# Optimization experiments

Measured on AMD Instinct MI355X. Metric: run time of the kernel, lower is better.

## Reference

```python
import jax, jax.numpy as jnp
import numpy as np

DMODEL = 1024
NHEADS = 16
FFN = 4 * DMODEL
HEAD_DIM = DMODEL // NHEADS
SCALE = HEAD_DIM ** -0.5


def layer_norm(x, gamma, beta, eps=1e-5):
    mu = jnp.mean(x, axis=-1, keepdims=True)
    var = jnp.var(x, axis=-1, keepdims=True)
    return (x - mu) * jax.lax.rsqrt(var + eps) * gamma + beta


def setup_inputs() -> dict:
    key = jax.random.key(0)
    ks = jax.random.split(key, 8)
    std = 0.02
    B, S = 2, 2048
    return {
        "src": jax.random.normal(ks[0], (B, S, DMODEL), jnp.float32),
        "pre_gamma": jnp.ones((DMODEL,), jnp.float32),
        "pre_beta": jnp.zeros((DMODEL,), jnp.float32),
        "qkv_w": jax.random.truncated_normal(ks[1], -2.0, 2.0, (3 * DMODEL, DMODEL), jnp.float32) * std,
        "qkv_b": jnp.zeros((3 * DMODEL,), jnp.float32),
        "addnorm_gamma": jnp.ones((DMODEL,), jnp.float32),
        "addnorm_beta": jnp.zeros((DMODEL,), jnp.float32),
        "fc1_w": jax.random.truncated_normal(ks[2], -2.0, 2.0, (FFN, DMODEL), jnp.float32) * std,
        "fc1_b": jnp.zeros((FFN,), jnp.float32),
        "fc2_w": jax.random.truncated_normal(ks[3], -2.0, 2.0, (DMODEL, FFN), jnp.float32) * std,
        "fc2_b": jnp.zeros((DMODEL,), jnp.float32),
    }


def reference(src, pre_gamma, pre_beta, qkv_w, qkv_b, addnorm_gamma, addnorm_beta,
              fc1_w, fc1_b, fc2_w, fc2_b):
    B, S, D = src.shape
    # PreNorm
    x = layer_norm(src, pre_gamma, pre_beta)
    # MHSA (no output projection, matching source)
    qkv = x @ qkv_w.T + qkv_b  # [B,S,3D]
    q, k, v = jnp.split(qkv, 3, axis=-1)
    def heads(t):
        return t.reshape(B, S, NHEADS, HEAD_DIM).transpose(0, 2, 1, 3)  # [B,H,S,hd]
    q, k, v = heads(q), heads(k), heads(v)
    attn = jnp.einsum("bhqd,bhkd->bhqk", q, k) * SCALE
    attn = jax.nn.softmax(attn, axis=-1)
    attn_out = jnp.einsum("bhqk,bhkd->bhqd", attn, v)
    attn_out = attn_out.transpose(0, 2, 1, 3).reshape(B, S, D)
    # shared AddNorm #1
    x = layer_norm(attn_out + x, addnorm_gamma, addnorm_beta)
    # FFN
    h = jax.nn.gelu(x @ fc1_w.T + fc1_b, approximate=False)
    ffn_out = h @ fc2_w.T + fc2_b
    # shared AddNorm #2 (same params as #1)
    return layer_norm(ffn_out + x, addnorm_gamma, addnorm_beta)
```

## Files before the change

kernel.cpp:

```cpp
#include <hip/hip_runtime.h>
#include <hip/hip_bf16.h>
#include <math.h>

#define DMODEL 1024
#define NH 16
#define HD 64
#define SEQ 2048
#define BATCH 2
#define MROWS (BATCH * SEQ)
#define FFN_DIM 4096

using bf16x8 = __attribute__((ext_vector_type(8))) __bf16;
using f32x4  = __attribute__((ext_vector_type(4))) float;

typedef const __attribute__((address_space(1))) unsigned char* gas_t;
typedef __attribute__((address_space(3))) unsigned char* las_t;

__device__ inline unsigned short f2bf(float f) {
    unsigned int u = __builtin_bit_cast(unsigned int, f);
    u += 0x7fffu + ((u >> 16) & 1u);
    return (unsigned short)(u >> 16);
}
__device__ inline unsigned short f2bf_up(float f) {
    unsigned int u = __builtin_bit_cast(unsigned int, f);
    return (unsigned short)((u + 0x8000u) >> 16);
}
__device__ inline float bf2f(unsigned short u) {
    unsigned int v = ((unsigned int)u) << 16;
    return __builtin_bit_cast(float, v);
}
__device__ inline float gelu_f(float x) {
    float x2 = x * x;
    float w = x * fmaf(0.07135481627f, x2, 1.59576912161f);
    return x / (1.0f + __expf(-w));
}

__global__ __launch_bounds__(256) void ln_pre_cvt(
        const float* __restrict__ a,
        const float* __restrict__ gamma, const float* __restrict__ beta,
        float* __restrict__ out_f, unsigned short* __restrict__ out_b,
        const float* __restrict__ wa, unsigned short* __restrict__ oa, int na4,
        const float* __restrict__ wb, unsigned short* __restrict__ ob, int nb4,
        const float* __restrict__ wc, unsigned char* __restrict__ oc, int nc4) {
    int blk = blockIdx.x;
    int t = threadIdx.x;
    if (blk >= MROWS) {
        int i = (blk - MROWS) * 256 + t;
        if (i < na4) {
            float4 v = ((const float4*)wa)[i];
            ushort4 o;
            o.x = f2bf(v.x); o.y = f2bf(v.y); o.z = f2bf(v.z); o.w = f2bf(v.w);
            ((ushort4*)oa)[i] = o;
        } else if (i < na4 + nb4) {
            int j = i - na4;
            float4 v = ((const float4*)wb)[j];
            ushort4 o;
            o.x = f2bf(v.x); o.y = f2bf(v.y); o.z = f2bf(v.z); o.w = f2bf(v.w);
            ((ushort4*)ob)[j] = o;
        } else if (i < na4 + nb4 + nc4) {
            int j = i - na4 - nb4;
            float4 v = ((const float4*)wc)[j];
            int pk = __builtin_amdgcn_cvt_pk_fp8_f32(v.x, v.y, 0, false);
            pk     = __builtin_amdgcn_cvt_pk_fp8_f32(v.z, v.w, pk, true);
            ((unsigned int*)oc)[j] = (unsigned int)pk;
        }
        return;
    }
    int row = blk;
    float4 v = ((const float4*)(a + (size_t)row * DMODEL))[t];
    float s  = v.x + v.y + v.z + v.w;
    float s2 = v.x * v.x + v.y * v.y + v.z * v.z + v.w * v.w;
    #pragma unroll
    for (int off = 32; off > 0; off >>= 1) {
        s  += __shfl_xor(s,  off, 64);
        s2 += __shfl_xor(s2, off, 64);
    }
    __shared__ float red[8];
    int wave = t >> 6, lane = t & 63;
    if (lane == 0) { red[wave] = s; red[4 + wave] = s2; }
    __syncthreads();
    float tot  = red[0] + red[1] + red[2] + red[3];
    float tot2 = red[4] + red[5] + red[6] + red[7];
    float mu   = tot * (1.0f / DMODEL);
    float var  = tot2 * (1.0f / DMODEL) - mu * mu;
    float rstd = rsqrtf(var + 1e-5f);
    float4 g  = ((const float4*)gamma)[t];
    float4 be = ((const float4*)beta)[t];
    float4 o;
    o.x = (v.x - mu) * rstd * g.x + be.x;
    o.y = (v.y - mu) * rstd * g.y + be.y;
    o.z = (v.z - mu) * rstd * g.z + be.z;
    o.w = (v.w - mu) * rstd * g.w + be.w;
    ((float4*)(out_f + (size_t)row * DMODEL))[t] = o;
    ushort4 ob4;
    ob4.x = f2bf(o.x); ob4.y = f2bf(o.y); ob4.z = f2bf(o.z); ob4.w = f2bf(o.w);
    ((ushort4*)(out_b + (size_t)row * DMODEL))[t] = ob4;
}

__global__ __launch_bounds__(256) void ln_attn(
        const float* __restrict__ o0, const float* __restrict__ o1,
        const float* __restrict__ l0, const float* __restrict__ l1,
        const float* __restrict__ xres,
        const float* __restrict__ gamma, const float* __restrict__ beta,
        float* __restrict__ out_f, unsigned short* __restrict__ out_b) {
    int row = blockIdx.x;
    int t = threadIdx.x;
    int b_ = row >> 11, s = row & 2047;
    int h = t >> 4;
    int bh = b_ * NH + h;
    size_t obase = ((size_t)bh * SEQ + s) * HD + (4 * t & 63);
    float4 va = ((const float4*)(o0 + obase))[0];
    float4 vb = ((const float4*)(o1 + obase))[0];
    float inv_l = 1.0f / (l0[(size_t)bh * SEQ + s] + l1[(size_t)bh * SEQ + s]);
    float4 rr = ((const float4*)(xres + (size_t)row * DMODEL))[t];
    float4 v;
    v.x = (va.x + vb.x) * inv_l + rr.x;
    v.y = (va.y + vb.y) * inv_l + rr.y;
    v.z = (va.z + vb.z) * inv_l + rr.z;
    v.w = (va.w + vb.w) * inv_l + rr.w;

    float s1 = v.x + v.y + v.z + v.w;
    float s2 = v.x * v.x + v.y * v.y + v.z * v.z + v.w * v.w;
    #pragma unroll
    for (int off = 32; off > 0; off >>= 1) {
        s1 += __shfl_xor(s1, off, 64);
        s2 += __shfl_xor(s2, off, 64);
    }
    __shared__ float red[8];
    int wave = t >> 6, lane = t & 63;
    if (lane == 0) { red[wave] = s1; red[4 + wave] = s2; }
    __syncthreads();
    float tot  = red[0] + red[1] + red[2] + red[3];
    float tot2 = red[4] + red[5] + red[6] + red[7];
    float mu   = tot * (1.0f / DMODEL);
    float var  = tot2 * (1.0f / DMODEL) - mu * mu;
    float rstd = rsqrtf(var + 1e-5f);
    float4 g  = ((const float4*)gamma)[t];
    float4 be = ((const float4*)beta)[t];
    float4 o;
    o.x = (v.x - mu) * rstd * g.x + be.x;
    o.y = (v.y - mu) * rstd * g.y + be.y;
    o.z = (v.z - mu) * rstd * g.z + be.z;
    o.w = (v.w - mu) * rstd * g.w + be.w;
    ((float4*)(out_f + (size_t)row * DMODEL))[t] = o;
    ushort4 ob;
    ob.x = f2bf(o.x); ob.y = f2bf(o.y); ob.z = f2bf(o.z); ob.w = f2bf(o.w);
    ((ushort4*)(out_b + (size_t)row * DMODEL))[t] = ob;
}

__global__ __launch_bounds__(256) void ln_fc2(
        const unsigned short* __restrict__ p0, const unsigned short* __restrict__ p1,
        const unsigned short* __restrict__ p2, const unsigned short* __restrict__ p3,
        const float* __restrict__ bias, const float* __restrict__ resid,
        const float* __restrict__ gamma, const float* __restrict__ beta,
        float* __restrict__ out_f) {
    int row = blockIdx.x;
    int t = threadIdx.x;
    size_t base = (size_t)row * DMODEL;
    ushort4 u0 = ((const ushort4*)(p0 + base))[t];
    ushort4 u1 = ((const ushort4*)(p1 + base))[t];
    ushort4 u2 = ((const ushort4*)(p2 + base))[t];
    ushort4 u3 = ((const ushort4*)(p3 + base))[t];
    float4 bb = ((const float4*)bias)[t];
    float4 rr = ((const float4*)(resid + base))[t];
    float4 v;
    v.x = bf2f(u0.x) + bf2f(u1.x) + bf2f(u2.x) + bf2f(u3.x) + bb.x + rr.x;
    v.y = bf2f(u0.y) + bf2f(u1.y) + bf2f(u2.y) + bf2f(u3.y) + bb.y + rr.y;
    v.z = bf2f(u0.z) + bf2f(u1.z) + bf2f(u2.z) + bf2f(u3.z) + bb.z + rr.z;
    v.w = bf2f(u0.w) + bf2f(u1.w) + bf2f(u2.w) + bf2f(u3.w) + bb.w + rr.w;

    float s  = v.x + v.y + v.z + v.w;
    float s2 = v.x * v.x + v.y * v.y + v.z * v.z + v.w * v.w;
    #pragma unroll
    for (int off = 32; off > 0; off >>= 1) {
        s  += __shfl_xor(s,  off, 64);
        s2 += __shfl_xor(s2, off, 64);
    }
    __shared__ float red[8];
    int wave = t >> 6, lane = t & 63;
    if (lane == 0) { red[wave] = s; red[4 + wave] = s2; }
    __syncthreads();
    float tot  = red[0] + red[1] + red[2] + red[3];
    float tot2 = red[4] + red[5] + red[6] + red[7];
    float mu   = tot * (1.0f / DMODEL);
    float var  = tot2 * (1.0f / DMODEL) - mu * mu;
    float rstd = rsqrtf(var + 1e-5f);
    float4 g  = ((const float4*)gamma)[t];
    float4 be = ((const float4*)beta)[t];
    float4 o;
    o.x = (v.x - mu) * rstd * g.x + be.x;
    o.y = (v.y - mu) * rstd * g.y + be.y;
    o.z = (v.z - mu) * rstd * g.z + be.z;
    o.w = (v.w - mu) * rstd * g.w + be.w;
    ((float4*)(out_f + base))[t] = o;
}

template <int MODE>
__global__ __launch_bounds__(256) void gemm_lds(
        const unsigned short* __restrict__ A,
        const unsigned short* __restrict__ Bw,
        const float* __restrict__ bias,
        void* __restrict__ out, int M, int N, int K) {
    __shared__ unsigned short As[2][128 * 64];
    __shared__ unsigned short Bs[2][128 * 64];

    const int tid  = threadIdx.x;
    const int wave = tid >> 6;
    const int lane = tid & 63;
    const int quad = lane >> 4;
    const int cc   = lane & 15;
    const int bn = blockIdx.x * 128;
    const int bm = blockIdx.y * 128;

    const unsigned short* Ab = A  + (size_t)bm * K;
    const unsigned short* Bb = Bw + (size_t)bn * K;

    const int srow0 = tid >> 3;
    const int sslot = tid & 7;
    const int rsw   = (cc >> 1) & 7;
    const int wm = (wave >> 1) * 64;
    const int wn = (wave & 1) * 64;

    f32x4 acc[4][4] = {};

    auto stage = [&](int buf, int k0) {
        #pragma unroll
        for (int i = 0; i < 4; ++i) {
            int row = i * 32 + srow0;
            int g   = sslot ^ ((row >> 1) & 7);
            const unsigned short* ga = Ab + (size_t)row * K + k0 + g * 8;
            const unsigned short* gb = Bb + (size_t)row * K + k0 + g * 8;
            unsigned short* la = &As[buf][i * 2048 + wave * 512];
            unsigned short* lb = &Bs[buf][i * 2048 + wave * 512];
            __builtin_amdgcn_global_load_lds((gas_t)(const void*)ga, (las_t)(void*)la, 16, 0, 0);
            __builtin_amdgcn_global_load_lds((gas_t)(const void*)gb, (las_t)(void*)lb, 16, 0, 0);
        }
    };

    const int nkt = K >> 6;
    stage(0, 0);
    __syncthreads();

    int cur = 0;
    for (int kt = 0; kt < nkt; ++kt) {
        if (kt + 1 < nkt) stage(cur ^ 1, (kt + 1) << 6);

        bf16x8 af[4][2], bf[4][2];
        #pragma unroll
        for (int mt = 0; mt < 4; ++mt)
            #pragma unroll
            for (int s = 0; s < 2; ++s) {
                int slot = (s * 4 + quad) ^ rsw;
                af[mt][s] = *(const bf16x8*)&As[cur][(wm + mt * 16 + cc) * 64 + slot * 8];
            }
        #pragma unroll
        for (int nt = 0; nt < 4; ++nt)
            #pragma unroll
            for (int s = 0; s < 2; ++s) {
                int slot = (s * 4 + quad) ^ rsw;
                bf[nt][s] = *(const bf16x8*)&Bs[cur][(wn + nt * 16 + cc) * 64 + slot * 8];
            }

        #pragma unroll
        for (int mt = 0; mt < 4; ++mt)
            #pragma unroll
            for (int nt = 0; nt < 4; ++nt) {
                acc[mt][nt] = __builtin_amdgcn_mfma_f32_16x16x32_bf16(
                    af[mt][0], bf[nt][0], acc[mt][nt], 0, 0, 0);
                acc[mt][nt] = __builtin_amdgcn_mfma_f32_16x16x32_bf16(
                    af[mt][1], bf[nt][1], acc[mt][nt], 0, 0, 0);
            }

        if (kt + 1 < nkt) __syncthreads();
        cur ^= 1;
    }

    #pragma unroll
    for (int mt = 0; mt < 4; ++mt)
        #pragma unroll
        for (int nt = 0; nt < 4; ++nt) {
            if constexpr (MODE == 1) {
                int m0 = bm + wm + mt * 16 + quad * 4;
                int n  = bn + wn + nt * 16 + cc;
                float bn_ = bias[n];
                float v0 = gelu_f(acc[mt][nt][0] + bn_);
                float v1 = gelu_f(acc[mt][nt][1] + bn_);
                float v2 = gelu_f(acc[mt][nt][2] + bn_);
                float v3 = gelu_f(acc[mt][nt][3] + bn_);
                int pk = __builtin_amdgcn_cvt_pk_fp8_f32(v0, v1, 0, false);
                pk     = __builtin_amdgcn_cvt_pk_fp8_f32(v2, v3, pk, true);
                unsigned char* o = (unsigned char*)out + (size_t)m0 * N + n;
                o[0]             = (unsigned char)pk;
                o[(size_t)N]     = (unsigned char)(pk >> 8);
                o[(size_t)2 * N] = (unsigned char)(pk >> 16);
                o[(size_t)3 * N] = (unsigned char)(pk >> 24);
            } else {
                #pragma unroll
                for (int r = 0; r < 4; ++r) {
                    int m = bm + wm + mt * 16 + quad * 4 + r;
                    int n = bn + wn + nt * 16 + cc;
                    float v = acc[mt][nt][r] + bias[n];
                    int b_ = m >> 11, srow = m & 2047;
                    int which = n >> 10, rem = n & 1023;
                    int h = rem >> 6, d = rem & 63;
                    if (which == 0) v *= 0.125f;
                    size_t idx = ((((size_t)which * BATCH + b_) * NH + h) * SEQ + srow) * HD + d;
                    ((unsigned short*)out)[idx] = f2bf(v);
                }
            }
        }
}

__global__ __launch_bounds__(256) void gemm_fp8(
        const unsigned char* __restrict__ A,
        const unsigned char* __restrict__ Bw,
        unsigned short* __restrict__ p0, unsigned short* __restrict__ p1,
        unsigned short* __restrict__ p2, unsigned short* __restrict__ p3,
        int M, int N, int K, int KC) {
    __shared__ unsigned char As[2][128 * 64];
    __shared__ unsigned char Bs[2][128 * 64];

    const int tid  = threadIdx.x;
    const int wave = tid >> 6;
    const int lane = tid & 63;
    const int quad = lane >> 4;
    const int cc   = lane & 15;
    const int bn = blockIdx.x * 128;
    const int bm = blockIdx.y * 128;

    const unsigned char* Ab = A  + (size_t)bm * K;
    const unsigned char* Bb = Bw + (size_t)bn * K;

    const int srow0 = tid >> 2;
    const int schunk = tid & 3;
    const int rsw = (cc >> 1) & 3;
    const int wm = (wave >> 1) * 64;
    const int wn = (wave & 1) * 64;

    const int kbeg = blockIdx.z * KC;

    f32x4 acc[4][4] = {};

    auto stage = [&](int buf, int k0) {
        #pragma unroll
        for (int i = 0; i < 2; ++i) {
            int row = i * 64 + srow0;
            int g   = schunk ^ ((row >> 1) & 3);
            const unsigned char* ga = Ab + (size_t)row * K + k0 + g * 16;
            const unsigned char* gb = Bb + (size_t)row * K + k0 + g * 16;
            unsigned char* la = &As[buf][i * 4096 + wave * 1024];
            unsigned char* lb = &Bs[buf][i * 4096 + wave * 1024];
            __builtin_amdgcn_global_load_lds((gas_t)(const void*)ga, (las_t)(void*)la, 16, 0, 0);
            __builtin_amdgcn_global_load_lds((gas_t)(const void*)gb, (las_t)(void*)lb, 16, 0, 0);
        }
    };

    const int nkt = KC >> 6;
    stage(0, kbeg);
    __syncthreads();

    int cur = 0;
    for (int kt = 0; kt < nkt; ++kt) {
        if (kt + 1 < nkt) stage(cur ^ 1, kbeg + ((kt + 1) << 6));

        long af[4][2], bf[4][2];
        #pragma unroll
        for (int mt = 0; mt < 4; ++mt)
            #pragma unroll
            for (int s = 0; s < 2; ++s) {
                int slot = ((quad >> 1) + 2 * s) ^ rsw;
                af[mt][s] = *(const long*)&As[cur][(wm + mt * 16 + cc) * 64 + slot * 16 + (quad & 1) * 8];
            }
        #pragma unroll
        for (int nt = 0; nt < 4; ++nt)
            #pragma unroll
            for (int s = 0; s < 2; ++s) {
                int slot = ((quad >> 1) + 2 * s) ^ rsw;
                bf[nt][s] = *(const long*)&Bs[cur][(wn + nt * 16 + cc) * 64 + slot * 16 + (quad & 1) * 8];
            }

        #pragma unroll
        for (int mt = 0; mt < 4; ++mt)
            #pragma unroll
            for (int nt = 0; nt < 4; ++nt) {
                acc[mt][nt] = __builtin_amdgcn_mfma_f32_16x16x32_fp8_fp8(
                    af[mt][0], bf[nt][0], acc[mt][nt], 0, 0, 0);
                acc[mt][nt] = __builtin_amdgcn_mfma_f32_16x16x32_fp8_fp8(
                    af[mt][1], bf[nt][1], acc[mt][nt], 0, 0, 0);
            }

        if (kt + 1 < nkt) __syncthreads();
        cur ^= 1;
    }

    unsigned short* outp = (blockIdx.z == 0) ? p0
                         : (blockIdx.z == 1) ? p1
                         : (blockIdx.z == 2) ? p2 : p3;
    #pragma unroll
    for (int mt = 0; mt < 4; ++mt)
        #pragma unroll
        for (int nt = 0; nt < 4; ++nt)
            #pragma unroll
            for (int r = 0; r < 4; ++r) {
                int m = bm + wm + mt * 16 + quad * 4 + r;
                int n = bn + wn + nt * 16 + cc;
                outp[(size_t)m * N + n] = f2bf(acc[mt][nt][r]);
            }
}

__global__ __launch_bounds__(256) void transpose_v(
        const unsigned short* __restrict__ vsrc, unsigned short* __restrict__ vt) {
    __shared__ unsigned short Ls[64 * 72];
    const int t = threadIdx.x;
    const int s0 = blockIdx.x * 64;
    const int bh = blockIdx.y;
    const unsigned short* in = vsrc + (size_t)bh * SEQ * HD;
    unsigned short* outp = vt + (size_t)bh * SEQ * HD;

    const int row = t >> 2;
    const int c8  = (t & 3) * 8;
    #pragma unroll
    for (int p = 0; p < 2; ++p)
        *(uint4*)&Ls[row * 72 + c8 + p * 32] =
            *(const uint4*)&in[(size_t)(s0 + row) * HD + c8 + p * 32];
    __syncthreads();

    const int hd = t >> 2;
    #pragma unroll
    for (int p = 0; p < 2; ++p) {
        unsigned short tmp[8];
        #pragma unroll
        for (int j = 0; j < 8; ++j)
            tmp[j] = Ls[(c8 + p * 32 + j) * 72 + hd];
        *(uint4*)&outp[(size_t)hd * SEQ + s0 + c8 + p * 32] = *(uint4*)tmp;
    }
}

#define KPAD 72
__global__ __launch_bounds__(256, 4) void attn_mfma(
        const unsigned short* __restrict__ qkv,
        const unsigned short* __restrict__ vt,
        float* __restrict__ op0, float* __restrict__ op1,
        float* __restrict__ lpart) {
    const int tid  = threadIdx.x;
    const int wave = tid >> 6;
    const int lane = tid & 63;
    const int quad = lane >> 4;
    const int cc   = lane & 15;
    const int qblk = blockIdx.x;
    const int bh   = blockIdx.y;
    const int half = blockIdx.z;

    const size_t headsz = (size_t)SEQ * HD;
    const unsigned short* qb  = qkv + (size_t)bh * headsz;
    const unsigned short* kb  = qkv + ((size_t)BATCH * NH + bh) * headsz;
    const unsigned short* vtb = vt + (size_t)bh * headsz;
    float* opart = half ? op1 : op0;
    float* lp    = lpart + (size_t)half * BATCH * NH * SEQ;

    __shared__ unsigned short Ks[64 * KPAD];
    __shared__ unsigned short Vt[64 * KPAD];
    __shared__ unsigned short Ps[4 * 32 * KPAD];

    bf16x8 qa[2][2];
    #pragma unroll
    for (int mt = 0; mt < 2; ++mt) {
        const unsigned short* qp =
            qb + (size_t)(qblk * 128 + wave * 32 + mt * 16 + cc) * HD + quad * 8;
        qa[mt][0] = *(const bf16x8*)qp;
        qa[mt][1] = *(const bf16x8*)(qp + 32);
    }

    f32x4 o_acc[2][4] = {};
    float l_i[2][4] = {};

    const int srow = wave * 16 + (lane >> 2);
    const int sc8  = (lane & 3) * 8;
    const int psw  = (cc >> 2) & 3;

    const int kt0 = half * 16, ktend = kt0 + 16;

    uint4 ka0, ka1, va0, va1;
    {
        const unsigned short* kp0 = &kb[(size_t)(kt0 * 64 + srow) * HD + sc8];
        const unsigned short* vp0 = &vtb[(size_t)srow * SEQ + kt0 * 64 + sc8];
        ka0 = *(const uint4*)kp0;
        ka1 = *(const uint4*)(kp0 + 32);
        va0 = *(const uint4*)vp0;
        va1 = *(const uint4*)(vp0 + 32);
    }

    for (int kt = kt0; kt < ktend; ++kt) {
        __syncthreads();
        *(uint4*)&Ks[srow * KPAD + sc8]      = ka0;
        *(uint4*)&Ks[srow * KPAD + sc8 + 32] = ka1;
        *(uint4*)&Vt[srow * KPAD + sc8]      = va0;
        *(uint4*)&Vt[srow * KPAD + sc8 + 32] = va1;
        __syncthreads();

        int ktn = (kt + 1 < ktend) ? kt + 1 : kt;
        const unsigned short* kpn = &kb[(size_t)(ktn * 64 + srow) * HD + sc8];
        const unsigned short* vpn = &vtb[(size_t)srow * SEQ + ktn * 64 + sc8];
        uint4 nk0 = *(const uint4*)kpn;
        uint4 nk1 = *(const uint4*)(kpn + 32);
        uint4 nv0 = *(const uint4*)vpn;
        uint4 nv1 = *(const uint4*)(vpn + 32);

        f32x4 s_acc[2][4];
        #pragma unroll
        for (int nt = 0; nt < 4; ++nt) {
            const unsigned short* kp = &Ks[(nt * 16 + cc) * KPAD + quad * 8];
            bf16x8 kf0 = *(const bf16x8*)kp;
            bf16x8 kf1 = *(const bf16x8*)(kp + 32);
            #pragma unroll
            for (int mt = 0; mt < 2; ++mt) {
                f32x4 z = {};
                z = __builtin_amdgcn_mfma_f32_16x16x32_bf16(qa[mt][0], kf0, z, 0, 0, 0);
                s_acc[mt][nt] = __builtin_amdgcn_mfma_f32_16x16x32_bf16(qa[mt][1], kf1, z, 0, 0, 0);
            }
        }

        unsigned short* pw = &Ps[wave * 32 * KPAD];
        #pragma unroll
        for (int mt = 0; mt < 2; ++mt)
            #pragma unroll
            for (int nt = 0; nt < 4; ++nt) {
                int pc = ((nt ^ quad) & 3) * 16 + cc;
                #pragma unroll
                for (int r = 0; r < 4; ++r) {
                    float e = __expf(s_acc[mt][nt][r]);
                    l_i[mt][r] += e;
                    pw[(mt * 16 + quad * 4 + r) * KPAD + pc] = f2bf_up(e);
                }
            }

        bf16x8 pf[2][2];
        #pragma unroll
        for (int mt = 0; mt < 2; ++mt) {
            const unsigned short* pa = &pw[(mt * 16 + cc) * KPAD];
            pf[mt][0] = *(const bf16x8*)&pa[((((quad >> 1))     ^ psw) & 3) * 16 + (quad & 1) * 8];
            pf[mt][1] = *(const bf16x8*)&pa[(((2 + (quad >> 1)) ^ psw) & 3) * 16 + (quad & 1) * 8];
        }

        #pragma unroll
        for (int nt = 0; nt < 4; ++nt) {
            const unsigned short* vp = &Vt[(nt * 16 + cc) * KPAD + quad * 8];
            bf16x8 vf0 = *(const bf16x8*)vp;
            bf16x8 vf1 = *(const bf16x8*)(vp + 32);
            #pragma unroll
            for (int mt = 0; mt < 2; ++mt) {
                o_acc[mt][nt] = __builtin_amdgcn_mfma_f32_16x16x32_bf16(
                    pf[mt][0], vf0, o_acc[mt][nt], 0, 0, 0);
                o_acc[mt][nt] = __builtin_amdgcn_mfma_f32_16x16x32_bf16(
                    pf[mt][1], vf1, o_acc[mt][nt], 0, 0, 0);
            }
        }

        ka0 = nk0; ka1 = nk1; va0 = nv0; va1 = nv1;
    }

    #pragma unroll
    for (int mt = 0; mt < 2; ++mt) {
        float lr[4];
        #pragma unroll
        for (int r = 0; r < 4; ++r) {
            float l = l_i[mt][r];
            #pragma unroll
            for (int off = 1; off < 16; off <<= 1)
                l += __shfl_xor(l, off, 64);
            lr[r] = l;
        }
        int rowbase = qblk * 128 + wave * 32 + mt * 16;
        if (cc == 0) {
            float4 lv = {lr[0], lr[1], lr[2], lr[3]};
            *(float4*)&lp[(size_t)bh * SEQ + rowbase + quad * 4] = lv;
        }
        #pragma unroll
        for (int nt = 0; nt < 4; ++nt)
            #pragma unroll
            for (int r = 0; r < 4; ++r) {
                int row = rowbase + quad * 4 + r;
                opart[((size_t)bh * SEQ + row) * HD + nt * 16 + cc] = o_acc[mt][nt][r];
            }
    }
}

extern "C" void kernel_launch(void* const* d_in, const int* in_sizes, int n_in,
                              void* d_out, int out_size, void* d_ws, size_t ws_size,
                              hipStream_t stream) {
    const float* src       = (const float*)d_in[0];
    const float* pre_gamma = (const float*)d_in[1];
    const float* pre_beta  = (const float*)d_in[2];
    const float* qkv_w     = (const float*)d_in[3];
    const float* qkv_b     = (const float*)d_in[4];
    const float* an_gamma  = (const float*)d_in[5];
    const float* an_beta   = (const float*)d_in[6];
    const float* fc1_w     = (const float*)d_in[7];
    const float* fc1_b     = (const float*)d_in[8];
    const float* fc2_w     = (const float*)d_in[9];
    const float* fc2_b     = (const float*)d_in[10];
    float* out = (float*)d_out;

    char* ws = (char*)d_ws;
    size_t off = 0;
    auto alloc = [&](size_t bytes) {
        char* p = ws + off;
        off += (bytes + 255) & ~(size_t)255;
        return p;
    };
    float*          x_f   = (float*)alloc((size_t)MROWS * DMODEL * 4);
    unsigned short* x_b   = (unsigned short*)alloc((size_t)MROWS * DMODEL * 2);
    float*          y_f   = (float*)alloc((size_t)MROWS * DMODEL * 4);
    unsigned short* y_b   = (unsigned short*)alloc((size_t)MROWS * DMODEL * 2);
    float*          atf   = (float*)alloc((size_t)MROWS * DMODEL * 4);
    float*          fff   = (float*)alloc((size_t)MROWS * DMODEL * 4);
    unsigned short* qkvb  = (unsigned short*)alloc((size_t)3 * MROWS * DMODEL * 2);
    unsigned char*  h8    = (unsigned char*)alloc((size_t)MROWS * FFN_DIM * 2);
    unsigned short* wqkv  = (unsigned short*)alloc((size_t)3 * DMODEL * DMODEL * 2);
    unsigned short* wfc1  = (unsigned short*)alloc((size_t)FFN_DIM * DMODEL * 2);
    unsigned char*  wfc28 = (unsigned char*)alloc((size_t)DMODEL * FFN_DIM);

    unsigned short* vt_b = (unsigned short*)fff;
    float* opart0 = atf;
    float* opart1 = (float*)h8;
    float* lpart  = (float*)x_b;
    unsigned short* fc2p0 = (unsigned short*)fff;
    unsigned short* fc2p1 = (unsigned short*)x_f;
    unsigned short* fc2p2 = (unsigned short*)atf;
    unsigned short* fc2p3 = (unsigned short*)qkvb;

    int n_qkv4 = 3 * DMODEL * DMODEL / 4;
    int n_fc4  = FFN_DIM * DMODEL / 4;
    int cvt_blocks = (n_qkv4 + 2 * n_fc4 + 255) / 256;

    ln_pre_cvt<<<dim3(MROWS + cvt_blocks), dim3(256), 0, stream>>>(
        src, pre_gamma, pre_beta, x_f, x_b,
        qkv_w, wqkv, n_qkv4, fc1_w, wfc1, n_fc4, fc2_w, wfc28, n_fc4);

    gemm_lds<3><<<dim3(3 * DMODEL / 128, MROWS / 128), dim3(256), 0, stream>>>(
        x_b, wqkv, qkv_b, qkvb, MROWS, 3 * DMODEL, DMODEL);
    transpose_v<<<dim3(SEQ / 64, BATCH * NH), dim3(256), 0, stream>>>(
        qkvb + (size_t)2 * BATCH * NH * SEQ * HD, vt_b);
    attn_mfma<<<dim3(SEQ / 128, BATCH * NH, 2), dim3(256), 0, stream>>>(
        qkvb, vt_b, opart0, opart1, lpart);
    ln_attn<<<dim3(MROWS), dim3(256), 0, stream>>>(
        opart0, opart1, lpart, lpart + (size_t)BATCH * NH * SEQ,
        x_f, an_gamma, an_beta, y_f, y_b);
    gemm_lds<1><<<dim3(FFN_DIM / 128, MROWS / 128), dim3(256), 0, stream>>>(
        y_b, wfc1, fc1_b, h8, MROWS, FFN_DIM, DMODEL);
    gemm_fp8<<<dim3(DMODEL / 128, MROWS / 128, 4), dim3(256), 0, stream>>>(
        h8, wfc28, fc2p0, fc2p1, fc2p2, fc2p3, MROWS, DMODEL, FFN_DIM, 1024);
    ln_fc2<<<dim3(MROWS), dim3(256), 0, stream>>>(
        fc2p0, fc2p1, fc2p2, fc2p3, fc2_b, y_f, an_gamma, an_beta, out);
}
```

Baseline: 321.3 us.

## Triple-buffer FP8 GEMM loads and swizzle attention K/V shared layout

The FP8 GEMM moves from double to triple buffering. It prefetches two k-tiles ahead and replaces __syncthreads with explicit vmcnt waits plus raw barriers, so global loads overlap more with MFMA work. The attention kernel swaps its padded K/V shared-memory tiles for an unpadded 64-wide layout with an XOR swizzle on 16-byte chunks, aimed at avoiding bank conflicts while using less LDS. The costs are more LDS per block in the GEMM, which may lower occupancy, and hand-written waitcnt values that must match the number of outstanding loads.

```diff
diff --git a/kernel.cpp b/kernel.cpp
--- a/kernel.cpp
+++ b/kernel.cpp
@@ -317,8 +317,8 @@
         unsigned short* __restrict__ p0, unsigned short* __restrict__ p1,
         unsigned short* __restrict__ p2, unsigned short* __restrict__ p3,
         int M, int N, int K, int KC) {
-    __shared__ unsigned char As[2][128 * 64];
-    __shared__ unsigned char Bs[2][128 * 64];
+    __shared__ unsigned char As[3][128 * 64];
+    __shared__ unsigned char Bs[3][128 * 64];
 
     const int tid  = threadIdx.x;
     const int wave = tid >> 6;
@@ -357,11 +357,18 @@
 
     const int nkt = KC >> 6;
     stage(0, kbeg);
-    __syncthreads();
+    if (nkt > 1) {
+        stage(1, kbeg + 64);
+        asm volatile("s_waitcnt vmcnt(4)" ::: "memory");
+    } else {
+        asm volatile("s_waitcnt vmcnt(0)" ::: "memory");
+    }
+    __builtin_amdgcn_s_barrier();
 
     int cur = 0;
     for (int kt = 0; kt < nkt; ++kt) {
-        if (kt + 1 < nkt) stage(cur ^ 1, kbeg + ((kt + 1) << 6));
+        int pbuf = cur + 2; if (pbuf >= 3) pbuf -= 3;
+        if (kt + 2 < nkt) stage(pbuf, kbeg + ((kt + 2) << 6));
 
         long af[4][2], bf[4][2];
         #pragma unroll
@@ -389,8 +396,15 @@
                     af[mt][1], bf[nt][1], acc[mt][nt], 0, 0, 0);
             }
 
-        if (kt + 1 < nkt) __syncthreads();
-        cur ^= 1;
+        if (kt + 1 < nkt) {
+            asm volatile("s_waitcnt lgkmcnt(0)" ::: "memory");
+            if (kt + 2 < nkt)
+                asm volatile("s_waitcnt vmcnt(4)" ::: "memory");
+            else
+                asm volatile("s_waitcnt vmcnt(0)" ::: "memory");
+            __builtin_amdgcn_s_barrier();
+        }
+        cur = (cur < 2) ? cur + 1 : 0;
     }
 
     unsigned short* outp = (blockIdx.z == 0) ? p0
@@ -458,8 +472,8 @@
     float* opart = half ? op1 : op0;
     float* lp    = lpart + (size_t)half * BATCH * NH * SEQ;
 
-    __shared__ unsigned short Ks[64 * KPAD];
-    __shared__ unsigned short Vt[64 * KPAD];
+    __shared__ unsigned short Ks[64 * 64];
+    __shared__ unsigned short Vt[64 * 64];
     __shared__ unsigned short Ps[4 * 32 * KPAD];
 
     bf16x8 qa[2][2];
@@ -474,44 +488,46 @@
     f32x4 o_acc[2][4] = {};
     float l_i[2][4] = {};
 
-    const int srow = wave * 16 + (lane >> 2);
-    const int sc8  = (lane & 3) * 8;
-    const int psw  = (cc >> 2) & 3;
+    const int srow0 = wave * 16 + (lane >> 3);
+    const int sc8c  = lane & 7;
+    const int swz   = (sc8c ^ (lane >> 3)) * 8;
+    const int psw   = (cc >> 2) & 3;
+    const int rw7   = cc & 7;
 
     const int kt0 = half * 16, ktend = kt0 + 16;
 
     uint4 ka0, ka1, va0, va1;
     {
-        const unsigned short* kp0 = &kb[(size_t)(kt0 * 64 + srow) * HD + sc8];
-        const unsigned short* vp0 = &vtb[(size_t)srow * SEQ + kt0 * 64 + sc8];
+        const unsigned short* kp0 = &kb[(size_t)(kt0 * 64 + srow0) * HD + sc8c * 8];
+        const unsigned short* vp0 = &vtb[(size_t)srow0 * SEQ + kt0 * 64 + sc8c * 8];
         ka0 = *(const uint4*)kp0;
-        ka1 = *(const uint4*)(kp0 + 32);
+        ka1 = *(const uint4*)(kp0 + 8 * HD);
         va0 = *(const uint4*)vp0;
-        va1 = *(const uint4*)(vp0 + 32);
+        va1 = *(const uint4*)(vp0 + 8 * SEQ);
     }
 
     for (int kt = kt0; kt < ktend; ++kt) {
         __syncthreads();
-        *(uint4*)&Ks[srow * KPAD + sc8]      = ka0;
-        *(uint4*)&Ks[srow * KPAD + sc8 + 32] = ka1;
-        *(uint4*)&Vt[srow * KPAD + sc8]      = va0;
-        *(uint4*)&Vt[srow * KPAD + sc8 + 32] = va1;
+        *(uint4*)&Ks[srow0 * 64 + swz]        = ka0;
+        *(uint4*)&Ks[(srow0 + 8) * 64 + swz]  = ka1;
+        *(uint4*)&Vt[srow0 * 64 + swz]        = va0;
+        *(uint4*)&Vt[(srow0 + 8) * 64 + swz]  = va1;
         __syncthreads();
 
         int ktn = (kt + 1 < ktend) ? kt + 1 : kt;
-        const unsigned short* kpn = &kb[(size_t)(ktn * 64 + srow) * HD + sc8];
-        const unsigned short* vpn = &vtb[(size_t)srow * SEQ + ktn * 64 + sc8];
+        const unsigned short* kpn = &kb[(size_t)(ktn * 64 + srow0) * HD + sc8c * 8];
+        const unsigned short* vpn = &vtb[(size_t)srow0 * SEQ + ktn * 64 + sc8c * 8];
         uint4 nk0 = *(const uint4*)kpn;
-        uint4 nk1 = *(const uint4*)(kpn + 32);
+        uint4 nk1 = *(const uint4*)(kpn + 8 * HD);
         uint4 nv0 = *(const uint4*)vpn;
-        uint4 nv1 = *(const uint4*)(vpn + 32);
+        uint4 nv1 = *(const uint4*)(vpn + 8 * SEQ);
 
         f32x4 s_acc[2][4];
         #pragma unroll
         for (int nt = 0; nt < 4; ++nt) {
-            const unsigned short* kp = &Ks[(nt * 16 + cc) * KPAD + quad * 8];
-            bf16x8 kf0 = *(const bf16x8*)kp;
-            bf16x8 kf1 = *(const bf16x8*)(kp + 32);
+            const unsigned short* kp = &Ks[(nt * 16 + cc) * 64];
+            bf16x8 kf0 = *(const bf16x8*)&kp[(quad ^ rw7) * 8];
+            bf16x8 kf1 = *(const bf16x8*)&kp[((quad + 4) ^ rw7) * 8];
             #pragma unroll
             for (int mt = 0; mt < 2; ++mt) {
                 f32x4 z = {};
@@ -544,9 +560,9 @@
 
         #pragma unroll
         for (int nt = 0; nt < 4; ++nt) {
-            const unsigned short* vp = &Vt[(nt * 16 + cc) * KPAD + quad * 8];
-            bf16x8 vf0 = *(const bf16x8*)vp;
-            bf16x8 vf1 = *(const bf16x8*)(vp + 32);
+            const unsigned short* vp = &Vt[(nt * 16 + cc) * 64];
+            bf16x8 vf0 = *(const bf16x8*)&vp[(quad ^ rw7) * 8];
+            bf16x8 vf1 = *(const bf16x8*)&vp[((quad + 4) ^ rw7) * 8];
             #pragma unroll
             for (int mt = 0; mt < 2; ++mt) {
                 o_acc[mt][nt] = __builtin_amdgcn_mfma_f32_16x16x32_bf16(
```

After: 318.1 us. No clear change (-1.0%).
